# Kernel optimization log

Measured on AMD Instinct MI355X. Metric: run time of the kernel, lower is better.

## Reference

```python
import jax, jax.numpy as jnp
import numpy as np

NUM_STEPS = 151
DIRECT_PRED_WEIGHT = 1.0
CLASS_NUM_PER_BATCH = 64
BATCH_SUPPORT_NUM_PER_CLASS = 8
SUPPORT = CLASS_NUM_PER_BATCH * BATCH_SUPPORT_NUM_PER_CLASS  # 512
BATCH = 65536
TARGET = BATCH - SUPPORT  # 65024
NUM_CLASSES = 64


def setup_inputs() -> dict:
    key = jax.random.key(0)
    k1, k2, k3 = jax.random.split(key, 3)
    direct_cls_logits = jax.random.normal(k1, (TARGET, NUM_CLASSES), dtype=jnp.float32)
    # similarities in [0,1) subset of the [-1,1] histogram support
    inner_product = jax.random.uniform(k2, (TARGET, SUPPORT), dtype=jnp.float32)
    cls_labels = jax.random.randint(k3, (BATCH,), 0, NUM_CLASSES, dtype=jnp.int64)
    return {"direct_cls_logits": direct_cls_logits,
            "inner_product": inner_product,
            "cls_labels": cls_labels}


def reference(direct_cls_logits, inner_product, cls_labels):
    step = 2.0 / (NUM_STEPS - 1)          # histogram bin width
    tsize = NUM_STEPS                      # t = -1, -1+step, ..., 1
    half = (NUM_STEPS - 1) // 2            # index offset so t_k = -1 + k*step

    support_labels = cls_labels[:SUPPORT]
    target_labels = cls_labels[SUPPORT:]

    # direct classification loss (mean cross entropy)
    logp = jax.nn.log_softmax(direct_cls_logits, axis=-1)
    nll = -jnp.take_along_axis(logp, target_labels[:, None], axis=1)[:, 0]
    direct_loss = jnp.mean(nll) * DIRECT_PRED_WEIGHT

    # pairwise positive/negative masks, flattened over all pairs
    mask_pos = (support_labels[None, :] == target_labels[:, None]).reshape(-1)
    m_pos = mask_pos.astype(jnp.float32)
    m_neg = 1.0 - m_pos
    pos_num = m_pos.sum()
    neg_num = m_neg.sum()

    # soft histogram via linear-interpolation scatter-add.
    # Original: bin k (t_k = floor(s/step)*step) gets (s - t_k)/step,
    #           bin k+1 gets (t_{k+1} - s)/step; bin tsize is dropped.
    s = inner_product.reshape(-1)
    kf = jnp.floor(s / step)
    frac = s / step - kf                   # (s - t_k)/step in [0,1)
    k = (kf).astype(jnp.int32) + half      # bin index of floor node

    def soft_hist(m, size):
        h = jnp.zeros((tsize + 1,), dtype=jnp.float32)
        h = h.at[k].add(frac * m)
        h = h.at[k + 1].add((1.0 - frac) * m)
        return h[:tsize] / size

    hist_pos = soft_hist(m_pos, pos_num)
    hist_neg = soft_hist(m_neg, neg_num)

    # CDF of positive histogram (triangular-matrix trick == cumsum)
    hist_pos_cdf = jnp.cumsum(hist_pos)
    histo_loss = jnp.sum(hist_neg * hist_pos_cdf)

    return histo_loss, direct_loss
```

## Files before the change

kernel.cpp:

```cpp
#include <hip/hip_runtime.h>

#define SUPPORT 512
#define TARGET  65024
#define NCLS    64
#define NQUAD   (TARGET / 4)
#define GS_ROWS 64
#define GS_BLK  (TARGET / GS_ROWS)
#define PH_BLK  2032
#define DR_BLK  1024

struct Accum {
    float hist_fr_sp[8][80];
    float hist_cnt_sp[8][80];
    float sum_all[8];
    float nll_sum[8];
    float Ta[80];
    float Tb[80];
    float spos;
    float pos_num;
    int   cls_off[NCLS + 1];
    int   cls_col[SUPPORT];
};
#define ZERO_WORDS (8 * 80 * 2 + 8 + 8)

__device__ __forceinline__ void lds_fadd(float* p, float v) {
    __hip_atomic_fetch_add(p, v, __ATOMIC_RELAXED, __HIP_MEMORY_SCOPE_WORKGROUP);
}

__global__ void prep_kernel(const int* __restrict__ labels, Accum* ws) {
    __shared__ int sh_cnt[NCLS], sh_off[NCLS], cur[NCLS];
    const int t = threadIdx.x;
    int* wsi = (int*)ws;
    for (int i = t; i < ZERO_WORDS; i += 512) wsi[i] = 0;
    if (t < NCLS) { sh_cnt[t] = 0; cur[t] = 0; }
    __syncthreads();
    const int c = labels[t];
    atomicAdd(&sh_cnt[c], 1);
    __syncthreads();
    if (t == 0) {
        int o = 0;
        for (int i = 0; i < NCLS; ++i) { sh_off[i] = o; ws->cls_off[i] = o; o += sh_cnt[i]; }
        ws->cls_off[NCLS] = o;
    }
    __syncthreads();
    const int slot = atomicAdd(&cur[c], 1);
    ws->cls_col[sh_off[c] + slot] = t;
}

__global__ __launch_bounds__(256) void poshist_kernel(const float* __restrict__ ip,
                                                      const int* __restrict__ labels,
                                                      Accum* __restrict__ ws) {
    __shared__ float hfr[76][8];
    __shared__ float hcnt[76][8];
    __shared__ int   colL[SUPPORT];
    __shared__ int   offL[NCLS + 1];
    const int tid = threadIdx.x;
    for (int i = tid; i < 76 * 8; i += 256) {
        (&hfr[0][0])[i] = 0.0f;
        (&hcnt[0][0])[i] = 0.0f;
    }
    for (int i = tid; i < SUPPORT; i += 256) colL[i] = ws->cls_col[i];
    if (tid <= NCLS) offL[tid] = ws->cls_off[tid];
    __syncthreads();

    const int row = (blockIdx.x * 256 + tid) >> 3;
    const int sl  = tid & 7;
    {
        const int c    = labels[SUPPORT + row];
        const int base = offL[c];
        const int cnt  = offL[c + 1] - base;
        const float* rptr = ip + (size_t)row * SUPPORT;
        for (int j = sl; j < cnt; j += 8) {
            const float s  = rptr[colL[base + j]];
            const float u  = s * 75.0f;
            const float fl = floorf(u);
            const int idx  = (int)fl;
            lds_fadd(&hfr[idx][sl],  u - fl);
            lds_fadd(&hcnt[idx][sl], 1.0f);
        }
    }
    __syncthreads();
    if (tid < 76) {
        float a = 0.0f, b = 0.0f;
        #pragma unroll
        for (int r = 0; r < 8; ++r) { a += hfr[tid][r]; b += hcnt[tid][r]; }
        if (a != 0.0f) unsafeAtomicAdd(&ws->hist_fr_sp[blockIdx.x & 7][tid], a);
        if (b != 0.0f) unsafeAtomicAdd(&ws->hist_cnt_sp[blockIdx.x & 7][tid], b);
    }
}

__global__ void cdf_kernel(Accum* ws) {
    __shared__ float Sfr[80], Cnt[80];
    const int t = threadIdx.x;
    if (t < 76) {
        float a = 0.0f, b = 0.0f;
        #pragma unroll
        for (int r = 0; r < 8; ++r) { a += ws->hist_fr_sp[r][t]; b += ws->hist_cnt_sp[r][t]; }
        Sfr[t] = a; Cnt[t] = b;
    }
    if (t >= 76 && t < 80) { Sfr[t] = 0.0f; Cnt[t] = 0.0f; }
    __syncthreads();
    if (t == 0) {
        float prevS = 0.0f, prevN = 0.0f, cacc = 0.0f;
        double sp = 0.0, pn = 0.0;
        for (int i = 0; i <= 76; ++i) {
            const float Si = (i < 76) ? Sfr[i] : 0.0f;
            const float Ni = (i < 76) ? Cnt[i] : 0.0f;
            const float Hi = Si + prevN - prevS;
            cacc += Hi;
            if (i >= 1) {
                const int k = i - 1;
                ws->Ta[k] = cacc + (float)k * Hi;
                ws->Tb[k] = Hi;
                sp += (double)prevN * cacc - (double)prevS * Hi;
            }
            pn += (double)Ni;
            prevS = Si; prevN = Ni;
        }
        for (int i = 77; i < 80; ++i) { ws->Ta[i] = 0.0f; ws->Tb[i] = 0.0f; }
        ws->spos = (float)sp;
        ws->pos_num = (float)pn;
    }
}

__global__ __launch_bounds__(256, 4) void stream_kernel(const float* __restrict__ ip,
                                                        const float* __restrict__ logits,
                                                        const int* __restrict__ labels,
                                                        Accum* __restrict__ ws) {
    __shared__ float2 tab[76 * 16];
    __shared__ float red[8];
    const int tid = threadIdx.x;

    if (blockIdx.x >= GS_BLK) {
        const int bid  = blockIdx.x - GS_BLK;
        const int wid  = tid >> 6;
        const int lane = tid & 63;
        const int sub  = lane >> 4;
        const int grpb = lane & ~15;

        float lsum = 0.0f;
        for (int q = bid * 4 + wid; q < NQUAD; q += DR_BLK * 4) {
            const float4 x = reinterpret_cast<const float4*>(logits)[q * 64 + lane];
            const int lab  = labels[SUPPORT + q * 4 + sub];
            float m = fmaxf(fmaxf(x.x, x.y), fmaxf(x.z, x.w));
            #pragma unroll
            for (int off = 1; off < 16; off <<= 1) m = fmaxf(m, __shfl_xor(m, off));
            float e = __expf(x.x - m) + __expf(x.y - m) + __expf(x.z - m) + __expf(x.w - m);
            #pragma unroll
            for (int off = 1; off < 16; off <<= 1) e += __shfl_xor(e, off);
            const int l3 = lab & 3;
            const float sel = l3 == 0 ? x.x : l3 == 1 ? x.y : l3 == 2 ? x.z : x.w;
            const float xl = __shfl(sel, grpb + (lab >> 2));
            if ((lane & 15) == 0) lsum += m + __logf(e) - xl;
        }
        #pragma unroll
        for (int off = 1; off < 64; off <<= 1) lsum += __shfl_xor(lsum, off);
        if (lane == 0) red[wid] = lsum;
        __syncthreads();
        if (tid == 0)
            unsafeAtomicAdd(&ws->nll_sum[bid & 7], red[0] + red[1] + red[2] + red[3]);
        return;
    }

    const int c16 = tid & 15;
    for (int i = tid; i < 76 * 16; i += 256)
        tab[i] = make_float2(ws->Ta[i >> 4], ws->Tb[i >> 4]);
    __syncthreads();

    const float4* base = reinterpret_cast<const float4*>(ip)
                       + (size_t)blockIdx.x * (GS_ROWS * 128) + tid;

    float sa0 = 0.0f, sb0 = 0.0f, sa1 = 0.0f, sb1 = 0.0f;
    float4 qa0, qa1, qa2, qa3, qa4, qa5, qa6, qa7;
    float4 qb0, qb1, qb2, qb3, qb4, qb5, qb6, qb7;

#define LDA(T) { qa0 = base[((T)+0)*256]; qa1 = base[((T)+1)*256]; \
                 qa2 = base[((T)+2)*256]; qa3 = base[((T)+3)*256]; \
                 qa4 = base[((T)+4)*256]; qa5 = base[((T)+5)*256]; \
                 qa6 = base[((T)+6)*256]; qa7 = base[((T)+7)*256]; }
#define LDB(T) { qb0 = base[((T)+0)*256]; qb1 = base[((T)+1)*256]; \
                 qb2 = base[((T)+2)*256]; qb3 = base[((T)+3)*256]; \
                 qb4 = base[((T)+4)*256]; qb5 = base[((T)+5)*256]; \
                 qb6 = base[((T)+6)*256]; qb7 = base[((T)+7)*256]; }
#define PE(S, SA, SB) { const float u = (S) * 75.0f; const int idx = (int)u;   \
                        const float2 ab = tab[(idx << 4) + c16];               \
                        SA += ab.x; SB = fmaf(u, ab.y, SB); }
#define P1(Q) { PE(Q.x, sa0, sb0) PE(Q.y, sa1, sb1) PE(Q.z, sa0, sb0) PE(Q.w, sa1, sb1) }
#define PA()  { P1(qa0) P1(qa1) P1(qa2) P1(qa3) P1(qa4) P1(qa5) P1(qa6) P1(qa7) }
#define PB()  { P1(qb0) P1(qb1) P1(qb2) P1(qb3) P1(qb4) P1(qb5) P1(qb6) P1(qb7) }

    LDA(0);
    LDB(8);
    PA();  LDA(16);
    PB();  LDB(24);
    PA();
    PB();

#undef LDA
#undef LDB
#undef PE
#undef P1
#undef PA
#undef PB

    float s_all = (sa0 + sa1) - (sb0 + sb1);
    #pragma unroll
    for (int off = 1; off < 64; off <<= 1) s_all += __shfl_xor(s_all, off);
    if ((tid & 63) == 0) red[tid >> 6] = s_all;
    __syncthreads();
    if (tid == 0)
        unsafeAtomicAdd(&ws->sum_all[blockIdx.x & 7], red[0] + red[1] + red[2] + red[3]);
}

__global__ void final_kernel(const Accum* __restrict__ ws, float* __restrict__ out) {
    if (threadIdx.x == 0 && blockIdx.x == 0) {
        double S = 0.0, nll = 0.0;
        for (int i = 0; i < 8; ++i) {
            S   += (double)ws->sum_all[i];
            nll += (double)ws->nll_sum[i];
        }
        const double pos = (double)ws->pos_num;
        const double tot = (double)TARGET * (double)SUPPORT;
        out[0] = (float)((S - (double)ws->spos) / (pos * (tot - pos)));
        out[1] = (float)(nll / (double)TARGET);
    }
}

extern "C" void kernel_launch(void* const* d_in, const int* in_sizes, int n_in,
                              void* d_out, int out_size, void* d_ws, size_t ws_size,
                              hipStream_t stream) {
    const float* logits = (const float*)d_in[0];
    const float* ip     = (const float*)d_in[1];
    const int*   labels = (const int*)d_in[2];
    float* out = (float*)d_out;
    Accum* ws  = (Accum*)d_ws;

    prep_kernel<<<1, 512, 0, stream>>>(labels, ws);
    poshist_kernel<<<PH_BLK, 256, 0, stream>>>(ip, labels, ws);
    cdf_kernel<<<1, 128, 0, stream>>>(ws);
    stream_kernel<<<GS_BLK + DR_BLK, 256, 0, stream>>>(ip, logits, labels, ws);
    final_kernel<<<1, 64, 0, stream>>>(ws, out);
}
```

Before: 76.79 us.

## Merge CDF into stream kernel and move direct loss into poshist launch

Drops the single-block cdf_kernel. Every stream block now redundantly rebuilds the interpolation tables from the per-slice histograms in shared memory, and block 0 writes spos and pos_num. The direct cross-entropy blocks move from the stream launch into the positive-histogram launch, so that light gather kernel overlaps with the logits work and the stream launch becomes pure histogram streaming. This removes one launch and its serialization gap, at the cost of a serial 77-step scan on one thread in every stream block before streaming starts.

```diff
diff --git a/kernel.cpp b/kernel.cpp
--- a/kernel.cpp
+++ b/kernel.cpp
@@ -14,8 +14,6 @@
     float hist_cnt_sp[8][80];
     float sum_all[8];
     float nll_sum[8];
-    float Ta[80];
-    float Tb[80];
     float spos;
     float pos_num;
     int   cls_off[NCLS + 1];
@@ -47,92 +45,51 @@
     ws->cls_col[sh_off[c] + slot] = t;
 }
 
-__global__ __launch_bounds__(256) void poshist_kernel(const float* __restrict__ ip,
-                                                      const int* __restrict__ labels,
-                                                      Accum* __restrict__ ws) {
-    __shared__ float hfr[76][8];
-    __shared__ float hcnt[76][8];
-    __shared__ int   colL[SUPPORT];
-    __shared__ int   offL[NCLS + 1];
+__global__ __launch_bounds__(256) void phdir_kernel(const float* __restrict__ ip,
+                                                    const float* __restrict__ logits,
+                                                    const int* __restrict__ labels,
+                                                    Accum* __restrict__ ws) {
     const int tid = threadIdx.x;
-    for (int i = tid; i < 76 * 8; i += 256) {
-        (&hfr[0][0])[i] = 0.0f;
-        (&hcnt[0][0])[i] = 0.0f;
-    }
-    for (int i = tid; i < SUPPORT; i += 256) colL[i] = ws->cls_col[i];
-    if (tid <= NCLS) offL[tid] = ws->cls_off[tid];
-    __syncthreads();
-
-    const int row = (blockIdx.x * 256 + tid) >> 3;
-    const int sl  = tid & 7;
-    {
-        const int c    = labels[SUPPORT + row];
-        const int base = offL[c];
-        const int cnt  = offL[c + 1] - base;
-        const float* rptr = ip + (size_t)row * SUPPORT;
-        for (int j = sl; j < cnt; j += 8) {
-            const float s  = rptr[colL[base + j]];
-            const float u  = s * 75.0f;
-            const float fl = floorf(u);
-            const int idx  = (int)fl;
-            lds_fadd(&hfr[idx][sl],  u - fl);
-            lds_fadd(&hcnt[idx][sl], 1.0f);
-        }
-    }
-    __syncthreads();
-    if (tid < 76) {
-        float a = 0.0f, b = 0.0f;
-        #pragma unroll
-        for (int r = 0; r < 8; ++r) { a += hfr[tid][r]; b += hcnt[tid][r]; }
-        if (a != 0.0f) unsafeAtomicAdd(&ws->hist_fr_sp[blockIdx.x & 7][tid], a);
-        if (b != 0.0f) unsafeAtomicAdd(&ws->hist_cnt_sp[blockIdx.x & 7][tid], b);
-    }
-}
-
-__global__ void cdf_kernel(Accum* ws) {
-    __shared__ float Sfr[80], Cnt[80];
-    const int t = threadIdx.x;
-    if (t < 76) {
-        float a = 0.0f, b = 0.0f;
-        #pragma unroll
-        for (int r = 0; r < 8; ++r) { a += ws->hist_fr_sp[r][t]; b += ws->hist_cnt_sp[r][t]; }
-        Sfr[t] = a; Cnt[t] = b;
-    }
-    if (t >= 76 && t < 80) { Sfr[t] = 0.0f; Cnt[t] = 0.0f; }
-    __syncthreads();
-    if (t == 0) {
-        float prevS = 0.0f, prevN = 0.0f, cacc = 0.0f;
-        double sp = 0.0, pn = 0.0;
-        for (int i = 0; i <= 76; ++i) {
-            const float Si = (i < 76) ? Sfr[i] : 0.0f;
-            const float Ni = (i < 76) ? Cnt[i] : 0.0f;
-            const float Hi = Si + prevN - prevS;
-            cacc += Hi;
-            if (i >= 1) {
-                const int k = i - 1;
-                ws->Ta[k] = cacc + (float)k * Hi;
-                ws->Tb[k] = Hi;
-                sp += (double)prevN * cacc - (double)prevS * Hi;
+    if (blockIdx.x < PH_BLK) {
+        __shared__ float hfr[76][8];
+        __shared__ float hcnt[76][8];
+        __shared__ int   colL[SUPPORT];
+        __shared__ int   offL[NCLS + 1];
+        for (int i = tid; i < 76 * 8; i += 256) {
+            (&hfr[0][0])[i] = 0.0f;
+            (&hcnt[0][0])[i] = 0.0f;
+        }
+        for (int i = tid; i < SUPPORT; i += 256) colL[i] = ws->cls_col[i];
+        if (tid <= NCLS) offL[tid] = ws->cls_off[tid];
+        __syncthreads();
+
+        const int row = (blockIdx.x * 256 + tid) >> 3;
+        const int sl  = tid & 7;
+        {
+            const int c    = labels[SUPPORT + row];
+            const int base = offL[c];
+            const int cnt  = offL[c + 1] - base;
+            const float* rptr = ip + (size_t)row * SUPPORT;
+            for (int j = sl; j < cnt; j += 8) {
+                const float s  = rptr[colL[base + j]];
+                const float u  = s * 75.0f;
+                const float fl = floorf(u);
+                const int idx  = (int)fl;
+                lds_fadd(&hfr[idx][sl],  u - fl);
+                lds_fadd(&hcnt[idx][sl], 1.0f);
             }
-            pn += (double)Ni;
-            prevS = Si; prevN = Ni;
-        }
-        for (int i = 77; i < 80; ++i) { ws->Ta[i] = 0.0f; ws->Tb[i] = 0.0f; }
-        ws->spos = (float)sp;
-        ws->pos_num = (float)pn;
-    }
-}
-
-__global__ __launch_bounds__(256, 4) void stream_kernel(const float* __restrict__ ip,
-                                                        const float* __restrict__ logits,
-                                                        const int* __restrict__ labels,
-                                                        Accum* __restrict__ ws) {
-    __shared__ float2 tab[76 * 16];
-    __shared__ float red[8];
-    const int tid = threadIdx.x;
-
-    if (blockIdx.x >= GS_BLK) {
-        const int bid  = blockIdx.x - GS_BLK;
+        }
+        __syncthreads();
+        if (tid < 76) {
+            float a = 0.0f, b = 0.0f;
+            #pragma unroll
+            for (int r = 0; r < 8; ++r) { a += hfr[tid][r]; b += hcnt[tid][r]; }
+            if (a != 0.0f) unsafeAtomicAdd(&ws->hist_fr_sp[blockIdx.x & 7][tid], a);
+            if (b != 0.0f) unsafeAtomicAdd(&ws->hist_cnt_sp[blockIdx.x & 7][tid], b);
+        }
+    } else {
+        __shared__ float red[4];
+        const int bid  = blockIdx.x - PH_BLK;
         const int wid  = tid >> 6;
         const int lane = tid & 63;
         const int sub  = lane >> 4;
@@ -159,12 +116,48 @@
         __syncthreads();
         if (tid == 0)
             unsafeAtomicAdd(&ws->nll_sum[bid & 7], red[0] + red[1] + red[2] + red[3]);
-        return;
-    }
-
+    }
+}
+
+__global__ __launch_bounds__(256, 4) void stream_kernel(const float* __restrict__ ip,
+                                                        Accum* __restrict__ ws) {
+    __shared__ float2 tab[76 * 16];
+    __shared__ float Sfr[80], Cnt[80];
+    __shared__ float Atab[80], Btab[80];
+    __shared__ float red[4];
+    const int tid = threadIdx.x;
+
+    if (tid < 76) {
+        float a = 0.0f, b = 0.0f;
+        #pragma unroll
+        for (int r = 0; r < 8; ++r) { a += ws->hist_fr_sp[r][tid]; b += ws->hist_cnt_sp[r][tid]; }
+        Sfr[tid] = a; Cnt[tid] = b;
+    }
+    if (tid >= 76 && tid < 80) { Sfr[tid] = 0.0f; Cnt[tid] = 0.0f; }
+    __syncthreads();
+    if (tid == 0) {
+        float prevS = 0.0f, prevN = 0.0f, cacc = 0.0f;
+        double sp = 0.0, pn = 0.0;
+        for (int i = 0; i <= 76; ++i) {
+            const float Si = (i < 76) ? Sfr[i] : 0.0f;
+            const float Ni = (i < 76) ? Cnt[i] : 0.0f;
+            const float Hi = Si + prevN - prevS;
+            cacc += Hi;
+            if (i >= 1) {
+                const int k = i - 1;
+                Atab[k] = cacc + (float)k * Hi;
+                Btab[k] = Hi;
+                sp += (double)prevN * cacc - (double)prevS * Hi;
+            }
+            pn += (double)Ni;
+            prevS = Si; prevN = Ni;
+        }
+        if (blockIdx.x == 0) { ws->spos = (float)sp; ws->pos_num = (float)pn; }
+    }
+    __syncthreads();
     const int c16 = tid & 15;
     for (int i = tid; i < 76 * 16; i += 256)
-        tab[i] = make_float2(ws->Ta[i >> 4], ws->Tb[i >> 4]);
+        tab[i] = make_float2(Atab[i >> 4], Btab[i >> 4]);
     __syncthreads();
 
     const float4* base = reinterpret_cast<const float4*>(ip)
@@ -236,8 +229,7 @@
     Accum* ws  = (Accum*)d_ws;
 
     prep_kernel<<<1, 512, 0, stream>>>(labels, ws);
-    poshist_kernel<<<PH_BLK, 256, 0, stream>>>(ip, labels, ws);
-    cdf_kernel<<<1, 128, 0, stream>>>(ws);
-    stream_kernel<<<GS_BLK + DR_BLK, 256, 0, stream>>>(ip, logits, labels, ws);
+    phdir_kernel<<<PH_BLK + DR_BLK, 256, 0, stream>>>(ip, logits, labels, ws);
+    stream_kernel<<<GS_BLK, 256, 0, stream>>>(ip, ws);
     final_kernel<<<1, 64, 0, stream>>>(ws, out);
 }
```

Measured after the change: 73.87 us. 1.04x faster.
